# Optimization experiments

Hardware: AMD Instinct MI355X
Metric: run time of the kernel (lower is better)

## Reference

```python
import jax, jax.numpy as jnp
import numpy as np

MASK_FILL = -987654321.0


def rotate_every_two(x):
    # pairs (x0, x1) -> (-x1, x0), interleaved back along last dim
    x1 = x[..., 0::2]
    x2 = x[..., 1::2]
    return jnp.stack((-x2, x1), axis=-1).reshape(x.shape)


def setup_inputs() -> dict:
    key = jax.random.key(0)
    ks = jax.random.split(key, 6)
    b, n, dim = 64, 197, 768
    heads, dim_head = 12, 64
    inner = heads * dim_head
    x = jax.random.normal(ks[0], (b, n, dim), dtype=jnp.float32)
    pos_emb = jax.random.normal(ks[1], (1, n, dim_head), dtype=jnp.float32)
    w_qkv = jax.random.normal(ks[2], (dim, 3 * inner), dtype=jnp.float32) * (dim ** -0.5)
    scale = jnp.full((heads,), dim_head ** -0.5, dtype=jnp.float32)
    w_out = jax.random.normal(ks[3], (inner, dim), dtype=jnp.float32) * (inner ** -0.5)
    b_out = jnp.zeros((dim,), dtype=jnp.float32)
    return {"x": x, "pos_emb": pos_emb, "w_qkv": w_qkv, "scale": scale,
            "w_out": w_out, "b_out": b_out}


def reference(x, pos_emb, w_qkv, scale, w_out, b_out):
    b, n, dim = x.shape
    h = scale.shape[0]
    qkv = x @ w_qkv                         # [b, n, 3*inner]
    q, k, v = jnp.split(qkv, 3, axis=-1)
    dh = q.shape[-1] // h
    to_heads = lambda t: t.reshape(b, n, h, dh).transpose(0, 2, 1, 3)  # bhnd
    q, k, v = to_heads(q), to_heads(k), to_heads(v)

    # RoPE: pos_emb [1, n, (2 * dh/2)] -> sin/cos [n, dh/2] -> interleave to [n, dh]
    sc = pos_emb[0].reshape(n, 2, dh // 2)
    sin = jnp.repeat(sc[:, 0], 2, axis=-1)  # [n, dh]
    cos = jnp.repeat(sc[:, 1], 2, axis=-1)
    q = q * cos + rotate_every_two(q) * sin
    k = k * cos + rotate_every_two(k) * sin

    # per-head learnable scale
    dots = jnp.einsum('bhid,bhjd->bhij', q, k) * scale[None, :, None, None]
    # diagonal (LSA) mask
    eye = jnp.eye(n, dtype=bool)
    dots = jnp.where(eye, MASK_FILL, dots)

    attn = jax.nn.softmax(dots, axis=-1)
    out = jnp.einsum('bhij,bhjd->bhid', attn, v)
    out = out.transpose(0, 2, 1, 3).reshape(b, n, h * dh)
    return out @ w_out + b_out
```

## Files before the change

kernel.cpp:

```cpp
#include <hip/hip_runtime.h>
#include <math.h>

#define MASK_FILL_F (-987654321.0f)

typedef unsigned short u16;
typedef unsigned int   u32;

constexpr int Bb   = 64;
constexpr int Ntok = 197;
constexpr int Dim  = 768;
constexpr int Heads= 12;
constexpr int Dh   = 64;
constexpr int Nq3  = 2304;
constexpr int Rows = 12608;
constexpr int Mpad = 12672;

using f32x4  = __attribute__((ext_vector_type(4))) float;
using bf16x8 = __attribute__((ext_vector_type(8))) short;

__device__ __forceinline__ u16 f2bf(float f) {
  u32 u = __float_as_uint(f);
  u = (u + 0x7fffu + ((u >> 16) & 1u)) >> 16;
  return (u16)u;
}

__device__ __forceinline__ void stage16(const void* gp, void* lp) {
  __builtin_amdgcn_global_load_lds(
      (const __attribute__((address_space(1))) u32*)gp,
      (__attribute__((address_space(3))) u32*)lp, 16, 0, 0);
}

__device__ __forceinline__ int sigma6(int M) {
  return (M & 0x23) | (((M >> 3) & 1) << 4) | (((M >> 2) & 1) << 3) |
         (((M >> 4) & 1) << 2);
}

__global__ __launch_bounds__(256) void cvt_bf16(const float* __restrict__ in,
                                                u16* __restrict__ out, int n4) {
  const int i = blockIdx.x * 256 + threadIdx.x;
  if (i < n4) {
    const float4 v = *(const float4*)&in[(size_t)i * 4];
    ushort4 u;
    u.x = f2bf(v.x); u.y = f2bf(v.y); u.z = f2bf(v.z); u.w = f2bf(v.w);
    *(ushort4*)&out[(size_t)i * 4] = u;
  }
}

__global__ __launch_bounds__(256) void transpose_cvt(const float* __restrict__ in,
                                                     u16* __restrict__ out,
                                                     int R, int C) {
  __shared__ float t[32][33];
  const int c0 = blockIdx.x * 32, r0 = blockIdx.y * 32;
  const int tx = threadIdx.x & 31, ty = threadIdx.x >> 5;
#pragma unroll
  for (int rr = ty; rr < 32; rr += 8)
    t[rr][tx] = in[(size_t)(r0 + rr) * C + c0 + tx];
  __syncthreads();
#pragma unroll
  for (int cc = ty; cc < 32; cc += 8)
    out[(size_t)(c0 + cc) * R + r0 + tx] = f2bf(t[tx][cc]);
}

__global__ __launch_bounds__(256) void vtrans(const u16* __restrict__ qkvB,
                                              u16* __restrict__ vT) {
  __shared__ u16 t[64 * 72];
  const int jt = blockIdx.x, bh = blockIdx.y;
  const int b = bh / Heads, h = bh % Heads;
  const int j0 = jt * 64;
  const int tid = threadIdx.x;

  for (int idx = tid; idx < 512; idx += 256) {
    const int jr = idx >> 3, c8 = (idx & 7) * 8;
    const int j = j0 + jr;
    uint4 u = make_uint4(0u, 0u, 0u, 0u);
    if (j < Ntok)
      u = *(const uint4*)(qkvB + (size_t)(b * Ntok + j) * Nq3 + 2 * Dim + h * Dh + c8);
    *(uint4*)&t[jr * 72 + c8] = u;
  }
  __syncthreads();
  for (int idx = tid; idx < 512; idx += 256) {
    const int d = idx >> 3, j8 = (idx & 7) * 8;
    ushort4 lo, hi;
    lo.x = t[(j8 + 0) * 72 + d]; lo.y = t[(j8 + 1) * 72 + d];
    lo.z = t[(j8 + 2) * 72 + d]; lo.w = t[(j8 + 3) * 72 + d];
    hi.x = t[(j8 + 4) * 72 + d]; hi.y = t[(j8 + 5) * 72 + d];
    hi.z = t[(j8 + 6) * 72 + d]; hi.w = t[(j8 + 7) * 72 + d];
    u16* dst = vT + ((size_t)bh * 64 + d) * 256 + j0 + j8;
    *(ushort4*)dst       = lo;
    *(ushort4*)(dst + 4) = hi;
  }
}

constexpr int Kc  = 768;
constexpr int NKT = Kc / 64;
#define KTC(x) ((x) < NKT ? (x) : (NKT - 1))

#define BARM() asm volatile("s_barrier" ::: "memory")
#define VMW4() asm volatile("s_waitcnt vmcnt(4)" ::: "memory")

#define STGA(chunk, kt, BUF) \
  stage16(Ag + (size_t)(m0 + (chunk) * 8 + srow) * Kc + (kt) * 64 + scol, \
          &As[BUF][(chunk) * 512])
#define STGB(chunk, kt, BUF) \
  stage16(Bg + (size_t)(n0 + (chunk) * 8 + srow) * Kc + (kt) * 64 + scol, \
          &Bs[BUF][(chunk) * 512])

#define RDA(BUF, MH) \
  _Pragma("unroll") for (int m_ = 0; m_ < 4; ++m_) \
  _Pragma("unroll") for (int k_ = 0; k_ < 2; ++k_) \
    af[m_][k_] = *(const bf16x8*)&As[BUF][(wr * 128 + (MH) * 64 + m_ * 16 + tx) * 64 \
                                          + (((k_ * 4 + qd) ^ sx) * 8)];
#define RDB(BUF, NH, BFR) \
  _Pragma("unroll") for (int n_ = 0; n_ < 2; ++n_) \
  _Pragma("unroll") for (int k_ = 0; k_ < 2; ++k_) \
    BFR[n_][k_] = *(const bf16x8*)&Bs[BUF][(wc * 64 + (NH) * 32 + n_ * 16 + tx) * 64 \
                                           + (((k_ * 4 + qd) ^ sx) * 8)];

#define MM(MH, NH, BFR) \
  __builtin_amdgcn_s_setprio(1); \
  _Pragma("unroll") for (int m_ = 0; m_ < 4; ++m_) \
  _Pragma("unroll") for (int n_ = 0; n_ < 2; ++n_) \
  _Pragma("unroll") for (int k_ = 0; k_ < 2; ++k_) \
    acc[(MH) * 4 + m_][(NH) * 2 + n_] = __builtin_amdgcn_mfma_f32_16x16x32_bf16( \
        af[m_][k_], BFR[n_][k_], acc[(MH) * 4 + m_][(NH) * 2 + n_], 0, 0, 0); \
  __builtin_amdgcn_s_setprio(0);

template<int TN>
__global__ __launch_bounds__(512, 2) void gemm8p(
    const u16* __restrict__ Ag, const u16* __restrict__ Bg,
    u16* __restrict__ Cb, int Nn, int nwg,
    const float* __restrict__ pe)
{
  __shared__ u16 As[2][256 * 64];
  __shared__ u16 Bs[2][256 * 64];

  const int tid = threadIdx.x, lane = tid & 63, w = tid >> 6;

  const int orig = blockIdx.x;
  const int q8 = nwg >> 3, r8 = nwg & 7;
  const int xcd = orig & 7, sub = orig >> 3;
  const int wgid = (xcd < r8 ? xcd * (q8 + 1) : r8 * (q8 + 1) + (xcd - r8) * q8) + sub;
  const int tm = wgid / TN, tn = wgid % TN;
  const int m0 = tm * 256, n0 = tn * 256;

  const int wr = w >> 2, wc = w & 3;
  const int tx = lane & 15, qd = lane >> 4, sx = tx & 7;

  const int srow = lane >> 3;
  const int scol = ((lane & 7) ^ srow) * 8;
  const int b0 = (w >> 1) * 8 + (w & 1) * 2;

  STGA(w, 0, 0);        STGA(16 + w, 0, 0);
  STGB(b0 + 4, 0, 0);   STGB(b0 + 5, 0, 0);
  STGA(8 + w, 0, 0);    STGA(24 + w, 0, 0);
  STGB(b0, 0, 0);       STGB(b0 + 1, 0, 0);
  STGA(w, 1, 1);        STGA(16 + w, 1, 1);
  STGB(b0 + 4, 1, 1);   STGB(b0 + 5, 1, 1);
  VMW4();
  BARM();

  f32x4  acc[8][4] = {};
  bf16x8 af[4][2], bf0[2][2], bf1[2][2];

#pragma unroll 1
  for (int i = 0; i < NKT / 2; ++i) {
    const int u = 2 * i;
    RDA(0, 0); RDB(0, 0, bf0);
    STGA(8 + w, u + 1, 1); STGA(24 + w, u + 1, 1);
    BARM(); MM(0, 0, bf0); BARM();
    RDB(0, 1, bf1);
    STGB(b0, u + 1, 1); STGB(b0 + 1, u + 1, 1);
    BARM(); MM(0, 1, bf1); BARM();
    RDA(0, 1);
    STGA(w, KTC(u + 2), 0); STGA(16 + w, KTC(u + 2), 0);
    BARM(); MM(1, 1, bf1); BARM();
    STGB(b0 + 4, KTC(u + 2), 0); STGB(b0 + 5, KTC(u + 2), 0);
    BARM(); MM(1, 0, bf0); VMW4(); BARM();
    RDA(1, 0); RDB(1, 0, bf0);
    STGA(8 + w, KTC(u + 2), 0); STGA(24 + w, KTC(u + 2), 0);
    BARM(); MM(0, 0, bf0); BARM();
    RDB(1, 1, bf1);
    STGB(b0, KTC(u + 2), 0); STGB(b0 + 1, KTC(u + 2), 0);
    BARM(); MM(0, 1, bf1); BARM();
    RDA(1, 1);
    STGA(w, KTC(u + 3), 1); STGA(16 + w, KTC(u + 3), 1);
    BARM(); MM(1, 1, bf1); BARM();
    STGB(b0 + 4, KTC(u + 3), 1); STGB(b0 + 5, KTC(u + 3), 1);
    BARM(); MM(1, 0, bf0); VMW4(); BARM();
  }

  const bool dorot = (n0 < 2 * Dim);
#pragma unroll
  for (int mi = 0; mi < 8; ++mi) {
    const int rbase = m0 + wr * 128 + mi * 16 + qd * 4;
    int iq[4];
#pragma unroll
    for (int r = 0; r < 4; ++r) iq[r] = (rbase + r) % Ntok;
#pragma unroll
    for (int ni = 0; ni < 4; ++ni) {
      const int col = n0 + wc * 64 + ni * 16 + tx;
      const int mm  = (col & 63) >> 1;
      const int odd = col & 1;
#pragma unroll
      for (int r = 0; r < 4; ++r) {
        float v = acc[mi][ni][r];
        float res = v;
        if (dorot) {
          const float other = __shfl_xor(v, 1, 64);
          const float sn = pe[iq[r] * 64 + mm];
          const float c2 = pe[iq[r] * 64 + 32 + mm];
          res = odd ? (v * c2 + other * sn) : (v * c2 - other * sn);
        }
        Cb[(size_t)(rbase + r) * Nn + col] = f2bf(res);
      }
    }
  }
}

__global__ __launch_bounds__(256) void gemm_bt1(
    const u16* __restrict__ Ag, const u16* __restrict__ Bg,
    float* __restrict__ C, int K, int Nn, const float* __restrict__ bias)
{
  __shared__ u16 As[128 * 32];
  __shared__ u16 Bs[128 * 32];
  const int tid = threadIdx.x, lane = tid & 63, w = tid >> 6;
  const int m0 = blockIdx.y * 128, n0 = blockIdx.x * 128;
  const int wm = (w & 1) * 64, wn = (w >> 1) * 64;
  const int tx = lane & 15, qk = lane >> 4;
  const int rs = lane >> 2, cs = (lane & 3) * 8;

  f32x4 acc[4][4] = {};

  for (int k0 = 0; k0 < K; k0 += 32) {
#pragma unroll
    for (int t = 0; t < 2; ++t) {
      const int r0 = w * 16 + t * 64;
      stage16(Ag + (size_t)(m0 + r0 + rs) * K + k0 + cs, &As[r0 * 32]);
      stage16(Bg + (size_t)(n0 + r0 + rs) * K + k0 + cs, &Bs[r0 * 32]);
    }
    __syncthreads();
    bf16x8 af[4], bf[4];
#pragma unroll
    for (int f = 0; f < 4; ++f) {
      af[f] = *(const bf16x8*)&As[(wm + f * 16 + tx) * 32 + qk * 8];
      bf[f] = *(const bf16x8*)&Bs[(wn + f * 16 + tx) * 32 + qk * 8];
    }
#pragma unroll
    for (int fm = 0; fm < 4; ++fm)
#pragma unroll
      for (int fn = 0; fn < 4; ++fn)
        acc[fm][fn] = __builtin_amdgcn_mfma_f32_16x16x32_bf16(
            af[fm], bf[fn], acc[fm][fn], 0, 0, 0);
    __syncthreads();
  }

#pragma unroll
  for (int fm = 0; fm < 4; ++fm) {
    const int rbase = m0 + wm + fm * 16 + qk * 4;
#pragma unroll
    for (int fn = 0; fn < 4; ++fn) {
      const int col = n0 + wn + fn * 16 + tx;
      const float bv = bias[col];
#pragma unroll
      for (int r = 0; r < 4; ++r) {
        const int row = rbase + r;
        if (row < Rows) C[(size_t)row * Nn + col] = acc[fm][fn][r] + bv;
      }
    }
  }
}

constexpr int LS = 72;

__global__ __launch_bounds__(1024) void attn16(
    const u16* __restrict__ qkvB, const u16* __restrict__ vT,
    const float* __restrict__ scale, u16* __restrict__ outB)
{
  __shared__ u16 ks [64 * LS];
  __shared__ u16 vts[64 * LS];

  const int bh = blockIdx.x;
  const int b = bh / Heads, h = bh % Heads;
  const float sc = scale[h];
  const int tid = threadIdx.x, lane = tid & 63, w = tid >> 6;
  const int tx = lane & 15, q = lane >> 4;
  const size_t rowbase = (size_t)b * Ntok;
  const bool active = (w < 13);

  const int Ms = (tid & 511) >> 3, c8s = (tid & 7) * 8;
  const bool isK = tid < 512;
  const u16* sgp = isK
      ? qkvB + (rowbase + sigma6(Ms)) * (size_t)Nq3 + Dim + h * Dh + c8s
      : vT + ((size_t)bh * 64 + Ms) * 256 + c8s;
  const size_t sstep = isK ? (size_t)64 * Nq3 : (size_t)64;
  u16* slds = (isK ? ks : vts) + Ms * LS + c8s;

  bf16x8 bq[2];
  if (active) {
#pragma unroll
    for (int kk = 0; kk < 2; ++kk)
      bq[kk] = *(const bf16x8*)(qkvB +
          (rowbase + 16 * w + tx) * (size_t)Nq3 + h * Dh + kk * 32 + q * 8);
  }

  uint4 sreg = *(const uint4*)sgp;

  float l_part = 0.f;
  f32x4 oacc[4] = {};

  for (int jt = 0; jt < 4; ++jt) {
    const int j0 = jt * 64;
    __syncthreads();
    *(uint4*)slds = sreg;
    __syncthreads();
    if (jt < 3) sreg = *(const uint4*)(sgp + (size_t)(jt + 1) * sstep);

    if (active) {
      f32x4 sT[4] = {};
      __builtin_amdgcn_s_setprio(1);
#pragma unroll
      for (int kk = 0; kk < 2; ++kk)
#pragma unroll
        for (int jb = 0; jb < 4; ++jb) {
          const bf16x8 ka = *(const bf16x8*)&ks[(jb * 16 + tx) * LS + kk * 32 + q * 8];
          sT[jb] = __builtin_amdgcn_mfma_f32_16x16x32_bf16(ka, bq[kk], sT[jb], 0, 0, 0);
        }
      __builtin_amdgcn_s_setprio(0);

      const int ig = 16 * w + tx;
      union { bf16x8 v; u16 e[8]; } pk[2];
      float lp = 0.f;
#pragma unroll
      for (int jb = 0; jb < 4; ++jb)
#pragma unroll
        for (int r = 0; r < 4; ++r) {
          const int jg = j0 + 32 * (jb >> 1) + 8 * q + 4 * (jb & 1) + r;
          const float s = fminf(sT[jb][r] * sc, 80.f);
          const bool bad = (jg >= Ntok) || (jg == ig);
          const float p = bad ? 0.f : __expf(s);
          lp += p;
          pk[jb >> 1].e[(jb & 1) * 4 + r] = f2bf(p);
        }
      l_part += lp;

      __builtin_amdgcn_s_setprio(1);
#pragma unroll
      for (int kk = 0; kk < 2; ++kk)
#pragma unroll
        for (int nb = 0; nb < 4; ++nb) {
          const bf16x8 vb = *(const bf16x8*)&vts[(nb * 16 + tx) * LS + kk * 32 + q * 8];
          oacc[nb] = __builtin_amdgcn_mfma_f32_16x16x32_bf16(pk[kk].v, vb,
                                                            oacc[nb], 0, 0, 0);
        }
      __builtin_amdgcn_s_setprio(0);
    }
  }

  if (active) {
    float l = l_part;
    l += __shfl_xor(l, 16, 64);
    l += __shfl_xor(l, 32, 64);
    const float linv = 1.0f / l;
#pragma unroll
    for (int r = 0; r < 4; ++r) {
      const float lr = __shfl(linv, 4 * q + r, 64);
      const int igr = 16 * w + 4 * q + r;
      if (igr < Ntok) {
#pragma unroll
        for (int nb = 0; nb < 4; ++nb)
          outB[(rowbase + igr) * (size_t)Dim + h * Dh + nb * 16 + tx] =
              f2bf(oacc[nb][r] * lr);
      }
    }
  }
}

extern "C" void kernel_launch(void* const* d_in, const int* in_sizes, int n_in,
                              void* d_out, int out_size, void* d_ws, size_t ws_size,
                              hipStream_t stream) {
  const float* x     = (const float*)d_in[0];
  const float* pe    = (const float*)d_in[1];
  const float* w_qkv = (const float*)d_in[2];
  const float* scale = (const float*)d_in[3];
  const float* w_out = (const float*)d_in[4];
  const float* b_out = (const float*)d_in[5];
  float* out = (float*)d_out;

  u16* xb    = (u16*)d_ws;
  u16* wqkvT = xb    + (size_t)Mpad * Dim;
  u16* woutT = wqkvT + (size_t)Nq3 * Dim;
  u16* qkvB  = woutT + (size_t)Dim * Dim;
  u16* attnB = qkvB  + (size_t)Mpad * Nq3;
  u16* vT    = attnB + (size_t)Mpad * Dim;

  cvt_bf16<<<(Rows * Dim / 4 + 255) / 256, 256, 0, stream>>>(x, xb, Rows * Dim / 4);
  transpose_cvt<<<dim3(Nq3 / 32, Dim / 32), 256, 0, stream>>>(w_qkv, wqkvT, Dim, Nq3);
  transpose_cvt<<<dim3(Dim / 32, Dim / 32), 256, 0, stream>>>(w_out, woutT, Dim, Dim);

  constexpr int NWG0 = 50 * 9;
  gemm8p<9><<<NWG0, 512, 0, stream>>>(xb, wqkvT, qkvB, Nq3, NWG0, pe);

  vtrans<<<dim3(4, Bb * Heads), 256, 0, stream>>>(qkvB, vT);

  attn16<<<Bb * Heads, 1024, 0, stream>>>(qkvB, vT, scale, attnB);

  gemm_bt1<<<dim3(Dim / 128, Mpad / 128), 256, 0, stream>>>(
      attnB, woutT, out, Dim, Dim, b_out);
}
```

Measured before the change: 273.3 us.

## Fuse input conversions into one prep kernel and transpose V inside attention

Merges the three conversion/transpose launches into a single prep kernel, using block-index ranges to select the work. Removes the separate vtrans kernel and its global vT buffer: V tiles are now loaded straight from qkvB into LDS and transposed in shared memory inside the attention kernel, with an extra barrier per tile. This cuts launch overhead and one global round trip for V, but adds LDS traffic, an extra buffer and a third barrier in each attention iteration.

```diff
diff --git a/kernel.cpp b/kernel.cpp
--- a/kernel.cpp
+++ b/kernel.cpp
@@ -35,23 +35,40 @@
          (((M >> 4) & 1) << 2);
 }
 
-__global__ __launch_bounds__(256) void cvt_bf16(const float* __restrict__ in,
-                                                u16* __restrict__ out, int n4) {
-  const int i = blockIdx.x * 256 + threadIdx.x;
-  if (i < n4) {
-    const float4 v = *(const float4*)&in[(size_t)i * 4];
-    ushort4 u;
-    u.x = f2bf(v.x); u.y = f2bf(v.y); u.z = f2bf(v.z); u.w = f2bf(v.w);
-    *(ushort4*)&out[(size_t)i * 4] = u;
-  }
-}
-
-__global__ __launch_bounds__(256) void transpose_cvt(const float* __restrict__ in,
-                                                     u16* __restrict__ out,
-                                                     int R, int C) {
+constexpr int NB_CVT = (Rows * Dim / 4 + 255) / 256;
+constexpr int NB_TQ  = (Nq3 / 32) * (Dim / 32);
+constexpr int NB_TO  = (Dim / 32) * (Dim / 32);
+
+__global__ __launch_bounds__(256) void prep(
+    const float* __restrict__ x, u16* __restrict__ xb,
+    const float* __restrict__ w_qkv, u16* __restrict__ wqkvT,
+    const float* __restrict__ w_out, u16* __restrict__ woutT)
+{
   __shared__ float t[32][33];
-  const int c0 = blockIdx.x * 32, r0 = blockIdx.y * 32;
-  const int tx = threadIdx.x & 31, ty = threadIdx.x >> 5;
+  const int bid = blockIdx.x, tid = threadIdx.x;
+
+  if (bid < NB_CVT) {
+    const int i = bid * 256 + tid;
+    if (i < Rows * Dim / 4) {
+      const float4 v = *(const float4*)&x[(size_t)i * 4];
+      ushort4 u;
+      u.x = f2bf(v.x); u.y = f2bf(v.y); u.z = f2bf(v.z); u.w = f2bf(v.w);
+      *(ushort4*)&xb[(size_t)i * 4] = u;
+    }
+    return;
+  }
+
+  const float* in; u16* out; int R, C, c0, r0;
+  if (bid < NB_CVT + NB_TQ) {
+    const int b2 = bid - NB_CVT;
+    in = w_qkv; out = wqkvT; R = Dim; C = Nq3;
+    c0 = (b2 % (Nq3 / 32)) * 32; r0 = (b2 / (Nq3 / 32)) * 32;
+  } else {
+    const int b3 = bid - NB_CVT - NB_TQ;
+    in = w_out; out = woutT; R = Dim; C = Dim;
+    c0 = (b3 % (Dim / 32)) * 32; r0 = (b3 / (Dim / 32)) * 32;
+  }
+  const int tx = tid & 31, ty = tid >> 5;
 #pragma unroll
   for (int rr = ty; rr < 32; rr += 8)
     t[rr][tx] = in[(size_t)(r0 + rr) * C + c0 + tx];
@@ -59,36 +76,6 @@
 #pragma unroll
   for (int cc = ty; cc < 32; cc += 8)
     out[(size_t)(c0 + cc) * R + r0 + tx] = f2bf(t[tx][cc]);
-}
-
-__global__ __launch_bounds__(256) void vtrans(const u16* __restrict__ qkvB,
-                                              u16* __restrict__ vT) {
-  __shared__ u16 t[64 * 72];
-  const int jt = blockIdx.x, bh = blockIdx.y;
-  const int b = bh / Heads, h = bh % Heads;
-  const int j0 = jt * 64;
-  const int tid = threadIdx.x;
-
-  for (int idx = tid; idx < 512; idx += 256) {
-    const int jr = idx >> 3, c8 = (idx & 7) * 8;
-    const int j = j0 + jr;
-    uint4 u = make_uint4(0u, 0u, 0u, 0u);
-    if (j < Ntok)
-      u = *(const uint4*)(qkvB + (size_t)(b * Ntok + j) * Nq3 + 2 * Dim + h * Dh + c8);
-    *(uint4*)&t[jr * 72 + c8] = u;
-  }
-  __syncthreads();
-  for (int idx = tid; idx < 512; idx += 256) {
-    const int d = idx >> 3, j8 = (idx & 7) * 8;
-    ushort4 lo, hi;
-    lo.x = t[(j8 + 0) * 72 + d]; lo.y = t[(j8 + 1) * 72 + d];
-    lo.z = t[(j8 + 2) * 72 + d]; lo.w = t[(j8 + 3) * 72 + d];
-    hi.x = t[(j8 + 4) * 72 + d]; hi.y = t[(j8 + 5) * 72 + d];
-    hi.z = t[(j8 + 6) * 72 + d]; hi.w = t[(j8 + 7) * 72 + d];
-    u16* dst = vT + ((size_t)bh * 64 + d) * 256 + j0 + j8;
-    *(ushort4*)dst       = lo;
-    *(ushort4*)(dst + 4) = hi;
-  }
 }
 
 constexpr int Kc  = 768;
@@ -273,11 +260,12 @@
 constexpr int LS = 72;
 
 __global__ __launch_bounds__(1024) void attn16(
-    const u16* __restrict__ qkvB, const u16* __restrict__ vT,
+    const u16* __restrict__ qkvB,
     const float* __restrict__ scale, u16* __restrict__ outB)
 {
-  __shared__ u16 ks [64 * LS];
-  __shared__ u16 vts[64 * LS];
+  __shared__ u16 ks  [64 * LS];
+  __shared__ u16 vtmp[64 * LS];
+  __shared__ u16 vts [64 * LS];
 
   const int bh = blockIdx.x;
   const int b = bh / Heads, h = bh % Heads;
@@ -289,11 +277,11 @@
 
   const int Ms = (tid & 511) >> 3, c8s = (tid & 7) * 8;
   const bool isK = tid < 512;
-  const u16* sgp = isK
-      ? qkvB + (rowbase + sigma6(Ms)) * (size_t)Nq3 + Dim + h * Dh + c8s
-      : vT + ((size_t)bh * 64 + Ms) * 256 + c8s;
-  const size_t sstep = isK ? (size_t)64 * Nq3 : (size_t)64;
-  u16* slds = (isK ? ks : vts) + Ms * LS + c8s;
+  const u16* kgp = qkvB + (rowbase + sigma6(Ms)) * (size_t)Nq3 + Dim + h * Dh + c8s;
+  const u16* vgp = qkvB + (rowbase + Ms) * (size_t)Nq3 + 2 * Dim + h * Dh + c8s;
+  u16* slds = (isK ? ks : vtmp) + Ms * LS + c8s;
+
+  const int td = tid & 63, tj8 = (tid & 511) >> 6;
 
   bf16x8 bq[2];
   if (active) {
@@ -303,7 +291,7 @@
           (rowbase + 16 * w + tx) * (size_t)Nq3 + h * Dh + kk * 32 + q * 8);
   }
 
-  uint4 sreg = *(const uint4*)sgp;
+  uint4 sreg = isK ? *(const uint4*)kgp : *(const uint4*)vgp;
 
   float l_part = 0.f;
   f32x4 oacc[4] = {};
@@ -313,7 +301,25 @@
     __syncthreads();
     *(uint4*)slds = sreg;
     __syncthreads();
-    if (jt < 3) sreg = *(const uint4*)(sgp + (size_t)(jt + 1) * sstep);
+
+    if (!isK) {
+      if (jt < 3) {
+        const int j = (jt + 1) * 64 + Ms;
+        sreg = (j < Ntok) ? *(const uint4*)(vgp + (size_t)(jt + 1) * 64 * Nq3)
+                          : make_uint4(0u, 0u, 0u, 0u);
+      }
+    } else {
+      ushort4 lo, hi;
+      lo.x = vtmp[(tj8 * 8 + 0) * LS + td]; lo.y = vtmp[(tj8 * 8 + 1) * LS + td];
+      lo.z = vtmp[(tj8 * 8 + 2) * LS + td]; lo.w = vtmp[(tj8 * 8 + 3) * LS + td];
+      hi.x = vtmp[(tj8 * 8 + 4) * LS + td]; hi.y = vtmp[(tj8 * 8 + 5) * LS + td];
+      hi.z = vtmp[(tj8 * 8 + 6) * LS + td]; hi.w = vtmp[(tj8 * 8 + 7) * LS + td];
+      *(ushort4*)&vts[td * LS + tj8 * 8]     = lo;
+      *(ushort4*)&vts[td * LS + tj8 * 8 + 4] = hi;
+      if (jt < 3)
+        sreg = *(const uint4*)(kgp + (size_t)(jt + 1) * 64 * Nq3);
+    }
+    __syncthreads();
 
     if (active) {
       f32x4 sT[4] = {};
@@ -391,18 +397,13 @@
   u16* woutT = wqkvT + (size_t)Nq3 * Dim;
   u16* qkvB  = woutT + (size_t)Dim * Dim;
   u16* attnB = qkvB  + (size_t)Mpad * Nq3;
-  u16* vT    = attnB + (size_t)Mpad * Dim;
-
-  cvt_bf16<<<(Rows * Dim / 4 + 255) / 256, 256, 0, stream>>>(x, xb, Rows * Dim / 4);
-  transpose_cvt<<<dim3(Nq3 / 32, Dim / 32), 256, 0, stream>>>(w_qkv, wqkvT, Dim, Nq3);
-  transpose_cvt<<<dim3(Dim / 32, Dim / 32), 256, 0, stream>>>(w_out, woutT, Dim, Dim);
+
+  prep<<<NB_CVT + NB_TQ + NB_TO, 256, 0, stream>>>(x, xb, w_qkv, wqkvT, w_out, woutT);
 
   constexpr int NWG0 = 50 * 9;
   gemm8p<9><<<NWG0, 512, 0, stream>>>(xb, wqkvT, qkvB, Nq3, NWG0, pe);
 
-  vtrans<<<dim3(4, Bb * Heads), 256, 0, stream>>>(qkvB, vT);
-
-  attn16<<<Bb * Heads, 1024, 0, stream>>>(qkvB, vT, scale, attnB);
+  attn16<<<Bb * Heads, 1024, 0, stream>>>(qkvB, scale, attnB);
 
   gemm_bt1<<<dim3(Dim / 128, Mpad / 128), 256, 0, stream>>>(
       attnB, woutT, out, Dim, Dim, b_out);
```

After: 262.2 us. -4.1%, faster.
